# Kernel optimization log

Hardware: AMD Instinct MI355X
Metric: run time of the kernel (lower is better)

The kernel has to match this reference:

```python
import jax, jax.numpy as jnp
import numpy as np

B, S, HID = 4, 2048, 1152
H, KV, D = 16, 8, 72
NDIM = 2
EPS = 1e-6


def rms_norm(x, w, eps=EPS):
    # Gemma-style: normalize in fp32, scale by (1 + w)
    var = jnp.mean(jnp.square(x.astype(jnp.float32)), axis=-1, keepdims=True)
    y = x.astype(jnp.float32) * jax.lax.rsqrt(var + eps)
    if w is not None:
        y = y * (1.0 + w.astype(jnp.float32))
    return y.astype(x.dtype)


def rotate_half(x):
    x1, x2 = jnp.split(x, 2, axis=-1)
    return jnp.concatenate([-x2, x1], axis=-1)


def multidim_rope(x, cos, sin, ndim=NDIM):
    # x: [B, S, h, D]; cos/sin: [B, S, D]; rotate per spatial axis on D//ndim chunks
    part = 2 * (x.shape[-1] // (2 * ndim))  # 36
    outs = []
    for i in range(ndim):
        sl = slice(i * part, (i + 1) * part)
        xp = x[..., sl]
        c = cos[..., sl][:, :, None, :]  # unsqueeze head dim
        s = sin[..., sl][:, :, None, :]
        outs.append(xp * c + rotate_half(xp) * s)
    return jnp.concatenate(outs, axis=-1)


def setup_inputs() -> dict:
    key = jax.random.key(0)
    ks = jax.random.split(key, 10)
    inv = 1.0 / np.sqrt(HID)
    return {
        "hidden_states": jax.random.normal(ks[0], (B, S, HID), jnp.float32),
        "cos": jax.random.uniform(ks[1], (B, S, D), jnp.float32),
        "sin": jax.random.uniform(ks[2], (B, S, D), jnp.float32),
        "attention_mask": jnp.zeros((B, 1, S, S), jnp.float32),
        "position_ids": jax.random.randint(ks[3], (B, S, NDIM), 0, 64, jnp.int32),
        "Wq": jax.random.normal(ks[4], (HID, H * D), jnp.float32) * inv,
        "Wk": jax.random.normal(ks[5], (HID, KV * D), jnp.float32) * inv,
        "Wv": jax.random.normal(ks[6], (HID, KV * D), jnp.float32) * inv,
        "Wo": jax.random.normal(ks[7], (H * D, HID), jnp.float32) * inv,
        "q_norm_w": jnp.zeros((D,), jnp.float32),
        "k_norm_w": jnp.zeros((D,), jnp.float32),
    }


def reference(hidden_states, cos, sin, attention_mask, position_ids,
              Wq, Wk, Wv, Wo, q_norm_w, k_norm_w):
    ndim = position_ids.shape[-1]
    groups = H // KV
    # projections -> [B, S, h, D]
    q = (hidden_states @ Wq).reshape(B, S, H, D)
    k = (hidden_states @ Wk).reshape(B, S, KV, D)
    v = (hidden_states @ Wv).reshape(B, S, KV, D)
    # per-head RMSNorm
    q = rms_norm(q, q_norm_w)
    k = rms_norm(k, k_norm_w)
    v = rms_norm(v, None)  # with_scale=False
    # split multidimensional RoPE
    q = multidim_rope(q, cos, sin, ndim)
    k = multidim_rope(k, cos, sin, ndim)
    # GQA: repeat kv heads
    k = jnp.repeat(k, groups, axis=2)  # [B, S, H, D]
    v = jnp.repeat(v, groups, axis=2)
    # attention (note: source applies NO 1/sqrt(D) scaling)
    scores = jnp.einsum("bqhd,bkhd->bhqk", q, k) + attention_mask
    probs = jax.nn.softmax(scores.astype(jnp.float32), axis=-1).astype(q.dtype)
    out = jnp.einsum("bhqk,bkhd->bqhd", probs, v).reshape(B, S, H * D)
    return out @ Wo
```

## Files before the change

### kernel.cpp

```cpp
#include <hip/hip_runtime.h>

typedef unsigned int u32;
typedef unsigned short u16;
typedef __attribute__((ext_vector_type(8))) short s8v;
typedef __attribute__((ext_vector_type(8))) __bf16 b8v;
typedef __attribute__((ext_vector_type(4))) float f4v;
typedef __attribute__((ext_vector_type(16))) float f32x16;
typedef __attribute__((ext_vector_type(4))) u32 u32x4;
typedef __attribute__((ext_vector_type(2))) u32 u32x2;

#define DEV static __device__ __forceinline__

DEV u32 cvtpk(float a, float b){ u32 r; asm("v_cvt_pk_bf16_f32 %0, %1, %2" : "=v"(r) : "v"(a), "v"(b)); return r; }
DEV u16 f2bf(float x){ return (u16)(cvtpk(x, x) & 0xffffu); }
DEV float bf2f(u16 u){ return __builtin_bit_cast(float, ((u32)u) << 16); }

DEV f4v mfma16(s8v a, s8v b, f4v c){
  return __builtin_amdgcn_mfma_f32_16x16x32_bf16(__builtin_bit_cast(b8v, a), __builtin_bit_cast(b8v, b), c, 0, 0, 0);
}
DEV f32x16 mfma32(s8v a, s8v b, f32x16 c){
  return __builtin_amdgcn_mfma_f32_32x32x16_bf16(__builtin_bit_cast(b8v, a), __builtin_bit_cast(b8v, b), c, 0, 0, 0);
}

DEV void gl_lds16(const void* g, void* l){
  __builtin_amdgcn_global_load_lds((const __attribute__((address_space(1))) u32*)g,
                                   (__attribute__((address_space(3))) u32*)l, 16, 0, 0);
}

__global__ __launch_bounds__(256) void k_prepx(const float* __restrict__ x, u16* __restrict__ xb, int n){
  int i = (blockIdx.x * 256 + threadIdx.x) * 8;
  if (i >= n) return;
  float4 a = *(const float4*)(x + i);
  float4 b = *(const float4*)(x + i + 4);
  u32x4 o;
  o.x = cvtpk(a.x, a.y); o.y = cvtpk(a.z, a.w);
  o.z = cvtpk(b.x, b.y); o.w = cvtpk(b.z, b.w);
  *(u32x4*)(xb + i) = o;
}

__global__ __launch_bounds__(256) void k_transpose(const float* __restrict__ src, u16* __restrict__ dst,
                                                   int K, int N, int ldd){
  __shared__ float t[32][33];
  int nt = N >> 5;
  int k0 = (blockIdx.x / nt) << 5, n0 = (blockIdx.x % nt) << 5;
  int col = threadIdx.x & 31, rw = threadIdx.x >> 5;
  #pragma unroll
  for (int i = 0; i < 4; i++){ int r = rw + i * 8; t[r][col] = src[(k0 + r) * N + n0 + col]; }
  __syncthreads();
  #pragma unroll
  for (int i = 0; i < 4; i++){ int r = rw + i * 8; dst[(n0 + r) * ldd + k0 + col] = f2bf(t[col][r]); }
}

template<int OUTF32>
__global__ __launch_bounds__(256) void k_gemm(const u16* __restrict__ A, const u16* __restrict__ Bt,
                                              void* __restrict__ Cv, int M, int N, int K){
  __shared__ u16 sA[128 * 64];
  __shared__ u16 sB[128 * 64];
  int tid = threadIdx.x, w = tid >> 6, lane = tid & 63, g = lane >> 4, c = lane & 15;
  int n0 = blockIdx.x << 7, m0 = blockIdx.y << 7;
  int wr = w >> 1, wc = w & 1;
  f4v acc[4][4] = {};
  int srow = lane >> 3;
  int sslot = (lane & 7) ^ srow;
  const u16* Abase = A + (m0 + srow) * K + sslot * 8;
  const u16* Bbase = Bt + (n0 + srow) * K + sslot * 8;
  #pragma unroll 1
  for (int kt = 0; kt < K; kt += 64){
    #pragma unroll
    for (int ii = 0; ii < 4; ii++){
      int i = w * 4 + ii;
      gl_lds16(Abase + i * 8 * K + kt, sA + i * 512);
      gl_lds16(Bbase + i * 8 * K + kt, sB + i * 512);
    }
    __syncthreads();
    #pragma unroll
    for (int kk = 0; kk < 2; kk++){
      s8v af[4], bfr[4];
      #pragma unroll
      for (int mi = 0; mi < 4; mi++){
        int r = (wr << 6) + (mi << 4) + c;
        int slot = ((kk << 2) + g) ^ (r & 7);
        af[mi] = *(const s8v*)(sA + r * 64 + slot * 8);
      }
      #pragma unroll
      for (int ni = 0; ni < 4; ni++){
        int r = (wc << 6) + (ni << 4) + c;
        int slot = ((kk << 2) + g) ^ (r & 7);
        bfr[ni] = *(const s8v*)(sB + r * 64 + slot * 8);
      }
      #pragma unroll
      for (int mi = 0; mi < 4; mi++)
        #pragma unroll
        for (int ni = 0; ni < 4; ni++)
          acc[mi][ni] = mfma16(af[mi], bfr[ni], acc[mi][ni]);
    }
    __syncthreads();
  }
  #pragma unroll
  for (int mi = 0; mi < 4; mi++){
    #pragma unroll
    for (int ni = 0; ni < 4; ni++){
      #pragma unroll
      for (int r = 0; r < 4; r++){
        int m = m0 + (wr << 6) + (mi << 4) + (g << 2) + r;
        int n = n0 + (wc << 6) + (ni << 4) + c;
        if (OUTF32) ((float*)Cv)[m * N + n] = acc[mi][ni][r];
        else        ((u16*)Cv)[m * N + n] = f2bf(acc[mi][ni][r]);
      }
    }
  }
}

__global__ __launch_bounds__(192) void k_normrope(const u16* __restrict__ Y, const float* __restrict__ cosp,
      const float* __restrict__ sinp, const float* __restrict__ qnw, const float* __restrict__ knw,
      u16* __restrict__ Qp, u16* __restrict__ Kp){
  __shared__ float ly[1728];
  int token = blockIdx.x;
  int t = threadIdx.x, head = t >> 3, j = t & 7;
  int base = head * 72 + j * 9;
  const u16* yr = Y + token * 2304;
  float x[9]; float ss = 0.f;
  #pragma unroll
  for (int i = 0; i < 9; i++){ x[i] = bf2f(yr[base + i]); ss += x[i] * x[i]; }
  ss += __shfl_xor(ss, 1); ss += __shfl_xor(ss, 2); ss += __shfl_xor(ss, 4);
  float inv = rsqrtf(ss * (1.f / 72.f) + 1e-6f);
  const float* wn = (head < 16) ? qnw : knw;
  #pragma unroll
  for (int i = 0; i < 9; i++){ int d = j * 9 + i; ly[base + i] = x[i] * inv * (1.f + wn[d]); }
  __syncthreads();
  const float* cs = cosp + token * 72;
  const float* sn = sinp + token * 72;
  float scale = (head < 16) ? 1.4426950408889634f : 1.0f;
  float o[9];
  #pragma unroll
  for (int i = 0; i < 9; i++){
    int d = j * 9 + i;
    int dm = (d >= 36) ? d - 36 : d;
    float rot = (dm < 18) ? -ly[head * 72 + d + 18] : ly[head * 72 + d - 18];
    o[i] = (ly[base + i] * cs[d] + rot * sn[d]) * scale;
  }
  int b = token >> 11, s = token & 2047;
  if (head < 16){
    u16* dst = Qp + (size_t)(((b << 4) + head) * 2048 + s) * 96;
    #pragma unroll
    for (int i = 0; i < 9; i++) dst[j * 9 + i] = f2bf(o[i]);
    #pragma unroll
    for (int p2 = 0; p2 < 3; p2++) dst[72 + j * 3 + p2] = 0;
  } else {
    u16* dst = Kp + (size_t)(((b << 3) + (head - 16)) * 2048 + s) * 128;
    #pragma unroll
    for (int i = 0; i < 9; i++) dst[j * 9 + i] = f2bf(o[i]);
    #pragma unroll
    for (int p2 = 0; p2 < 7; p2++) dst[72 + j * 7 + p2] = 0;
  }
}

__global__ __launch_bounds__(256) void k_vtrans(const u16* __restrict__ Y, u16* __restrict__ Vt){
  __shared__ float lv[72][33];
  int st = blockIdx.x, bk = blockIdx.y;
  int b = bk >> 3, kvh = bk & 7;
  int t = threadIdx.x, tl = t >> 3, j = t & 7;
  int token = (b << 11) + (st << 5) + tl;
  const u16* yr = Y + token * 2304 + 1728 + kvh * 72 + j * 9;
  float x[9]; float ss = 0.f;
  #pragma unroll
  for (int i = 0; i < 9; i++){ x[i] = bf2f(yr[i]); ss += x[i] * x[i]; }
  ss += __shfl_xor(ss, 1); ss += __shfl_xor(ss, 2); ss += __shfl_xor(ss, 4);
  float inv = rsqrtf(ss * (1.f / 72.f) + 1e-6f);
  #pragma unroll
  for (int i = 0; i < 9; i++) lv[j * 9 + i][tl] = x[i] * inv;
  __syncthreads();
  u16* vb = Vt + bk * 72 * 2048 + (st << 5);
  for (int e = t; e < 72 * 32; e += 256){
    int r = e >> 5, cl = e & 31;
    vb[r * 2048 + cl] = f2bf(lv[r][cl]);
  }
}

__global__ __launch_bounds__(512, 4) void k_attn(const u16* __restrict__ Qp, const u16* __restrict__ Kp,
                                                 const u16* __restrict__ Vt, u16* __restrict__ O){
  __shared__ u16 sK[2][64 * 128];
  __shared__ u16 sV[2][96 * 64];
  int tid = threadIdx.x, w = tid >> 6, lane = tid & 63, hi = lane >> 5, l31 = lane & 31;
  int qt = blockIdx.x, bh = blockIdx.y, b = bh >> 4, h = bh & 15, kv = h >> 1;
  int q = (qt << 8) + (w << 5) + l31;
  const u16* qb = Qp + (size_t)((((b << 4) + h) << 11) + q) * 96;
  s8v qf[5];
  #pragma unroll
  for (int ds = 0; ds < 5; ds++) qf[ds] = *(const s8v*)(qb + ds * 16 + hi * 8);
  f32x16 ao[3] = {};
  float mv = -3.0e38f, lsp = 0.f;
  const char* kb = (const char*)Kp + (((size_t)((b << 3) + kv)) << 11) * 256;
  const char* vb = (const char*)Vt + (size_t)((b << 3) + kv) * 72 * 4096;
  int kn0 = (0 * 8 + w) * 64 + lane, kn1 = (1 * 8 + w) * 64 + lane;
  int kr0 = kn0 >> 4, kr1 = kn1 >> 4;
  int ksrc0 = kr0 * 256 + (((lane & 15) ^ (kr0 & 15)) << 4);
  int ksrc1 = kr1 * 256 + (((lane & 15) ^ (kr1 & 15)) << 4);
  int kdst0 = kn0 << 4, kdst1 = kn1 << 4;
  int vn0 = w * 64 + lane, vn1 = 512 + lane;
  int vr0 = vn0 >> 3, vr1 = vn1 >> 3;
  int vsrc0 = vr0 * 4096 + (((lane & 7) ^ (vr0 & 7)) << 4);
  int vsrc1 = vr1 * 4096 + (((lane & 7) ^ (vr1 & 7)) << 4);
  int vdst0 = vn0 << 4, vdst1 = vn1 << 4;

#define STAGE_KV(buf, t1) { \
    const char* kt_ = kb + (size_t)(t1) * 16384; \
    gl_lds16(kt_ + ksrc0, (char*)sK[buf] + kdst0); \
    gl_lds16(kt_ + ksrc1, (char*)sK[buf] + kdst1); \
    const char* vt_ = vb + (size_t)(t1) * 128; \
    gl_lds16(vt_ + vsrc0, (char*)sV[buf] + vdst0); \
    if (w == 0) gl_lds16(vt_ + vsrc1, (char*)sV[buf] + vdst1); }

  STAGE_KV(0, 0)
  __syncthreads();

  #pragma unroll 1
  for (int t = 0; t < 32; t++){
    int cur = t & 1, nxt = cur ^ 1;
    if (t < 31){ STAGE_KV(nxt, t + 1) }
    const u16* sKc = sK[cur];
    f32x16 s0 = {}, s1 = {};
    __builtin_amdgcn_s_setprio(1);
    #pragma unroll
    for (int ds = 0; ds < 5; ds++){
      int s = ds * 2 + hi;
      int r0 = l31, r1 = 32 + l31;
      s8v k0 = *(const s8v*)(sKc + r0 * 128 + ((s ^ (r0 & 15)) << 3));
      s8v k1 = *(const s8v*)(sKc + r1 * 128 + ((s ^ (r1 & 15)) << 3));
      s0 = mfma32(k0, qf[ds], s0);
      s1 = mfma32(k1, qf[ds], s1);
    }
    __builtin_amdgcn_s_setprio(0);
    float tm = s0[0];
    #pragma unroll
    for (int i = 1; i < 16; i++) tm = fmaxf(tm, s0[i]);
    #pragma unroll
    for (int i = 0; i < 16; i++) tm = fmaxf(tm, s1[i]);
    tm = fmaxf(tm, __shfl_xor(tm, 32));
    if (!__all(tm <= mv + 8.f)){
      float mn = fmaxf(mv, tm);
      float scl = exp2f(mv - mn);
      lsp *= scl;
      ao[0] *= scl; ao[1] *= scl; ao[2] *= scl;
      mv = mn;
    }
    float ts = 0.f;
    #pragma unroll
    for (int i = 0; i < 16; i++){ float e = exp2f(s0[i] - mv); s0[i] = e; ts += e; }
    #pragma unroll
    for (int i = 0; i < 16; i++){ float e = exp2f(s1[i] - mv); s1[i] = e; ts += e; }
    lsp += ts;
    s8v pf[4];
#define MK_PF(S, ks) { \
      const int blo = ((ks) & 1) * 8; \
      u32 a0 = cvtpk(S[blo + 0], S[blo + 1]); \
      u32 a1 = cvtpk(S[blo + 2], S[blo + 3]); \
      u32 b0 = cvtpk(S[blo + 4], S[blo + 5]); \
      u32 b1 = cvtpk(S[blo + 6], S[blo + 7]); \
      asm("v_permlane32_swap_b32 %0, %1" : "+v"(a0), "+v"(b0)); \
      asm("v_permlane32_swap_b32 %0, %1" : "+v"(a1), "+v"(b1)); \
      u32x4 w4 = {a0, a1, b0, b1}; \
      pf[ks] = __builtin_bit_cast(s8v, w4); }
    MK_PF(s0, 0) MK_PF(s0, 1) MK_PF(s1, 2) MK_PF(s1, 3)
#undef MK_PF
    const u16* sVc = sV[cur];
    __builtin_amdgcn_s_setprio(1);
    #pragma unroll
    for (int ks = 0; ks < 4; ks++){
      int s = ks * 2 + hi;
      #pragma unroll
      for (int dt = 0; dt < 3; dt++){
        int r = dt * 32 + l31;
        s8v vf = *(const s8v*)(sVc + r * 64 + ((s ^ (r & 7)) << 3));
        ao[dt] = mfma32(vf, pf[ks], ao[dt]);
      }
    }
    __builtin_amdgcn_s_setprio(0);
    __syncthreads();
  }
  float ls = lsp + __shfl_xor(lsp, 32);
  float inv = 1.f / ls;
  u16* ob = O + (size_t)((((b << 11) + q) << 4) + h) * 72;
  #pragma unroll
  for (int dt = 0; dt < 3; dt++){
    #pragma unroll
    for (int gp = 0; gp < 4; gp++){
      int d = dt * 32 + gp * 8 + hi * 4;
      if (d < 72){
        u32x2 o2;
        o2.x = cvtpk(ao[dt][gp * 4 + 0] * inv, ao[dt][gp * 4 + 1] * inv);
        o2.y = cvtpk(ao[dt][gp * 4 + 2] * inv, ao[dt][gp * 4 + 3] * inv);
        *(u32x2*)(ob + d) = o2;
      }
    }
  }
#undef STAGE_KV
}

extern "C" void kernel_launch(void* const* d_in, const int* in_sizes, int n_in,
                              void* d_out, int out_size, void* d_ws, size_t ws_size,
                              hipStream_t stream){
  (void)in_sizes; (void)n_in; (void)out_size; (void)ws_size;
  const float* hs   = (const float*)d_in[0];
  const float* cosp = (const float*)d_in[1];
  const float* sinp = (const float*)d_in[2];
  const float* Wq   = (const float*)d_in[5];
  const float* Wk   = (const float*)d_in[6];
  const float* Wv   = (const float*)d_in[7];
  const float* Wo   = (const float*)d_in[8];
  const float* qnw  = (const float*)d_in[9];
  const float* knw  = (const float*)d_in[10];
  char* ws = (char*)d_ws;
  u16* Xb    = (u16*)(ws);
  u16* WtQKV = (u16*)(ws + 18874368);
  u16* Wot   = (u16*)(ws + 24182784);
  u16* Y     = (u16*)(ws + 26836992);
  u16* Qp    = (u16*)(ws + 64585728);
  u16* Kp    = (u16*)(ws + 89751552);
  u16* Vt    = (u16*)(ws + 106528768);
  u16* O     = Xb;

  k_prepx<<<4608, 256, 0, stream>>>(hs, Xb, 8192 * 1152);
  k_transpose<<<36 * 36, 256, 0, stream>>>(Wq, WtQKV, 1152, 1152, 1152);
  k_transpose<<<36 * 18, 256, 0, stream>>>(Wk, WtQKV + 1152 * 1152, 1152, 576, 1152);
  k_transpose<<<36 * 18, 256, 0, stream>>>(Wv, WtQKV + 1728 * 1152, 1152, 576, 1152);
  k_transpose<<<36 * 36, 256, 0, stream>>>(Wo, Wot, 1152, 1152, 1152);
  k_gemm<0><<<dim3(18, 64), 256, 0, stream>>>(Xb, WtQKV, Y, 8192, 2304, 1152);
  k_normrope<<<8192, 192, 0, stream>>>(Y, cosp, sinp, qnw, knw, Qp, Kp);
  k_vtrans<<<dim3(64, 32), 256, 0, stream>>>(Y, Vt);
  k_attn<<<dim3(8, 64), 512, 0, stream>>>(Qp, Kp, Vt, O);
  k_gemm<1><<<dim3(9, 64), 256, 0, stream>>>(O, Wot, (float*)d_out, 8192, 1152, 1152);
}
```

Before: 324.9 us.

## Share KV tiles across GQA head pair and double KV tile to 128

Each attention block now serves both query heads that share one KV head (4 waves per head, 128 queries each), so the staged K/V tiles in LDS are reused by two heads and global KV traffic halves. The KV tile grows from 64 to 128 keys per iteration, halving loop trips and barriers, with the LDS swizzle rewritten for 128-wide V rows. This raises LDS use and register pressure (four score accumulators), and launch bounds drop to 2 blocks per CU, which reduces occupancy.

```diff
diff --git a/kernel.cpp b/kernel.cpp
--- a/kernel.cpp
+++ b/kernel.cpp
@@ -177,65 +177,78 @@
   }
 }
 
-__global__ __launch_bounds__(512, 4) void k_attn(const u16* __restrict__ Qp, const u16* __restrict__ Kp,
+__global__ __launch_bounds__(512, 2) void k_attn(const u16* __restrict__ Qp, const u16* __restrict__ Kp,
                                                  const u16* __restrict__ Vt, u16* __restrict__ O){
-  __shared__ u16 sK[2][64 * 128];
-  __shared__ u16 sV[2][96 * 64];
+  __shared__ u16 sK[2][128 * 128];
+  __shared__ u16 sV[2][96 * 128];
   int tid = threadIdx.x, w = tid >> 6, lane = tid & 63, hi = lane >> 5, l31 = lane & 31;
-  int qt = blockIdx.x, bh = blockIdx.y, b = bh >> 4, h = bh & 15, kv = h >> 1;
-  int q = (qt << 8) + (w << 5) + l31;
+  int bk = blockIdx.x, qt = blockIdx.y;
+  int b = bk >> 3, kv = bk & 7;
+  int h = (kv << 1) + (w >> 2);
+  int q = (qt << 7) + ((w & 3) << 5) + l31;
   const u16* qb = Qp + (size_t)((((b << 4) + h) << 11) + q) * 96;
   s8v qf[5];
   #pragma unroll
   for (int ds = 0; ds < 5; ds++) qf[ds] = *(const s8v*)(qb + ds * 16 + hi * 8);
   f32x16 ao[3] = {};
   float mv = -3.0e38f, lsp = 0.f;
-  const char* kb = (const char*)Kp + (((size_t)((b << 3) + kv)) << 11) * 256;
-  const char* vb = (const char*)Vt + (size_t)((b << 3) + kv) * 72 * 4096;
-  int kn0 = (0 * 8 + w) * 64 + lane, kn1 = (1 * 8 + w) * 64 + lane;
-  int kr0 = kn0 >> 4, kr1 = kn1 >> 4;
-  int ksrc0 = kr0 * 256 + (((lane & 15) ^ (kr0 & 15)) << 4);
-  int ksrc1 = kr1 * 256 + (((lane & 15) ^ (kr1 & 15)) << 4);
-  int kdst0 = kn0 << 4, kdst1 = kn1 << 4;
-  int vn0 = w * 64 + lane, vn1 = 512 + lane;
-  int vr0 = vn0 >> 3, vr1 = vn1 >> 3;
-  int vsrc0 = vr0 * 4096 + (((lane & 7) ^ (vr0 & 7)) << 4);
-  int vsrc1 = vr1 * 4096 + (((lane & 7) ^ (vr1 & 7)) << 4);
-  int vdst0 = vn0 << 4, vdst1 = vn1 << 4;
-
-#define STAGE_KV(buf, t1) { \
-    const char* kt_ = kb + (size_t)(t1) * 16384; \
-    gl_lds16(kt_ + ksrc0, (char*)sK[buf] + kdst0); \
-    gl_lds16(kt_ + ksrc1, (char*)sK[buf] + kdst1); \
-    const char* vt_ = vb + (size_t)(t1) * 128; \
-    gl_lds16(vt_ + vsrc0, (char*)sV[buf] + vdst0); \
-    if (w == 0) gl_lds16(vt_ + vsrc1, (char*)sV[buf] + vdst1); }
-
-  STAGE_KV(0, 0)
+  const char* kb = (const char*)Kp + (size_t)bk * 2048 * 256;
+  const char* vb = (const char*)Vt + (size_t)bk * 72 * 4096;
+  int ko[4], kd[4];
+  #pragma unroll
+  for (int i = 0; i < 4; i++){
+    int n = (i * 8 + w) * 64 + lane;
+    int kr = n >> 4, sp = n & 15;
+    ko[i] = kr * 256 + ((sp ^ (kr & 15)) << 4);
+    kd[i] = n << 4;
+  }
+  int vo[3], vd[3];
+  #pragma unroll
+  for (int i = 0; i < 3; i++){
+    int n = (i < 2) ? (i * 512 + w * 64 + lane) : (1024 + w * 16 + (lane & 15));
+    int vr = n >> 4, sp = n & 15;
+    vo[i] = vr * 4096 + ((sp ^ (vr & 15)) << 4);
+    vd[i] = n << 4;
+  }
+
+#define STAGE(buf, t1) { \
+    const char* kt_ = kb + (size_t)(t1) * 32768; \
+    gl_lds16(kt_ + ko[0], (char*)sK[buf] + kd[0]); \
+    gl_lds16(kt_ + ko[1], (char*)sK[buf] + kd[1]); \
+    gl_lds16(kt_ + ko[2], (char*)sK[buf] + kd[2]); \
+    gl_lds16(kt_ + ko[3], (char*)sK[buf] + kd[3]); \
+    const char* vt_ = vb + (size_t)(t1) * 256; \
+    gl_lds16(vt_ + vo[0], (char*)sV[buf] + vd[0]); \
+    gl_lds16(vt_ + vo[1], (char*)sV[buf] + vd[1]); \
+    if (lane < 16) gl_lds16(vt_ + vo[2], (char*)sV[buf] + vd[2]); }
+
+  STAGE(0, 0)
   __syncthreads();
 
   #pragma unroll 1
-  for (int t = 0; t < 32; t++){
+  for (int t = 0; t < 16; t++){
     int cur = t & 1, nxt = cur ^ 1;
-    if (t < 31){ STAGE_KV(nxt, t + 1) }
+    if (t < 15){ STAGE(nxt, t + 1) }
     const u16* sKc = sK[cur];
-    f32x16 s0 = {}, s1 = {};
+    f32x16 sc[4];
     __builtin_amdgcn_s_setprio(1);
     #pragma unroll
-    for (int ds = 0; ds < 5; ds++){
-      int s = ds * 2 + hi;
-      int r0 = l31, r1 = 32 + l31;
-      s8v k0 = *(const s8v*)(sKc + r0 * 128 + ((s ^ (r0 & 15)) << 3));
-      s8v k1 = *(const s8v*)(sKc + r1 * 128 + ((s ^ (r1 & 15)) << 3));
-      s0 = mfma32(k0, qf[ds], s0);
-      s1 = mfma32(k1, qf[ds], s1);
+    for (int j = 0; j < 4; j++){
+      sc[j] = {};
+      int r = j * 32 + l31;
+      #pragma unroll
+      for (int ds = 0; ds < 5; ds++){
+        int s = ds * 2 + hi;
+        s8v kf = *(const s8v*)(sKc + r * 128 + ((s ^ (r & 15)) << 3));
+        sc[j] = mfma32(kf, qf[ds], sc[j]);
+      }
     }
     __builtin_amdgcn_s_setprio(0);
-    float tm = s0[0];
-    #pragma unroll
-    for (int i = 1; i < 16; i++) tm = fmaxf(tm, s0[i]);
-    #pragma unroll
-    for (int i = 0; i < 16; i++) tm = fmaxf(tm, s1[i]);
+    float tm = sc[0][0];
+    #pragma unroll
+    for (int j = 0; j < 4; j++)
+      #pragma unroll
+      for (int i = 0; i < 16; i++) tm = fmaxf(tm, sc[j][i]);
     tm = fmaxf(tm, __shfl_xor(tm, 32));
     if (!__all(tm <= mv + 8.f)){
       float mn = fmaxf(mv, tm);
@@ -244,38 +257,43 @@
       ao[0] *= scl; ao[1] *= scl; ao[2] *= scl;
       mv = mn;
     }
-    float ts = 0.f;
-    #pragma unroll
-    for (int i = 0; i < 16; i++){ float e = exp2f(s0[i] - mv); s0[i] = e; ts += e; }
-    #pragma unroll
-    for (int i = 0; i < 16; i++){ float e = exp2f(s1[i] - mv); s1[i] = e; ts += e; }
-    lsp += ts;
-    s8v pf[4];
-#define MK_PF(S, ks) { \
-      const int blo = ((ks) & 1) * 8; \
-      u32 a0 = cvtpk(S[blo + 0], S[blo + 1]); \
-      u32 a1 = cvtpk(S[blo + 2], S[blo + 3]); \
-      u32 b0 = cvtpk(S[blo + 4], S[blo + 5]); \
-      u32 b1 = cvtpk(S[blo + 6], S[blo + 7]); \
+    float ts0 = 0.f, ts1 = 0.f;
+    #pragma unroll
+    for (int j = 0; j < 4; j++){
+      #pragma unroll
+      for (int i = 0; i < 8; i++){ float e = exp2f(sc[j][i] - mv); sc[j][i] = e; ts0 += e; }
+      #pragma unroll
+      for (int i = 8; i < 16; i++){ float e = exp2f(sc[j][i] - mv); sc[j][i] = e; ts1 += e; }
+    }
+    lsp += ts0 + ts1;
+    const u16* sVc = sV[cur];
+#define MK_PF(S, mlo, PF) { \
+      u32 a0 = cvtpk(S[mlo + 0], S[mlo + 1]); \
+      u32 a1 = cvtpk(S[mlo + 2], S[mlo + 3]); \
+      u32 b0 = cvtpk(S[mlo + 4], S[mlo + 5]); \
+      u32 b1 = cvtpk(S[mlo + 6], S[mlo + 7]); \
       asm("v_permlane32_swap_b32 %0, %1" : "+v"(a0), "+v"(b0)); \
       asm("v_permlane32_swap_b32 %0, %1" : "+v"(a1), "+v"(b1)); \
       u32x4 w4 = {a0, a1, b0, b1}; \
-      pf[ks] = __builtin_bit_cast(s8v, w4); }
-    MK_PF(s0, 0) MK_PF(s0, 1) MK_PF(s1, 2) MK_PF(s1, 3)
-#undef MK_PF
-    const u16* sVc = sV[cur];
-    __builtin_amdgcn_s_setprio(1);
-    #pragma unroll
-    for (int ks = 0; ks < 4; ks++){
-      int s = ks * 2 + hi;
+      PF = __builtin_bit_cast(s8v, w4); }
+    #pragma unroll
+    for (int j = 0; j < 4; j++){
+      s8v pfa, pfb;
+      MK_PF(sc[j], 0, pfa)
+      MK_PF(sc[j], 8, pfb)
+      __builtin_amdgcn_s_setprio(1);
       #pragma unroll
       for (int dt = 0; dt < 3; dt++){
         int r = dt * 32 + l31;
-        s8v vf = *(const s8v*)(sVc + r * 64 + ((s ^ (r & 7)) << 3));
-        ao[dt] = mfma32(vf, pf[ks], ao[dt]);
-      }
-    }
-    __builtin_amdgcn_s_setprio(0);
+        int s0 = 4 * j + hi, s1 = 4 * j + 2 + hi;
+        s8v vf0 = *(const s8v*)(sVc + r * 128 + ((s0 ^ (r & 15)) << 3));
+        s8v vf1 = *(const s8v*)(sVc + r * 128 + ((s1 ^ (r & 15)) << 3));
+        ao[dt] = mfma32(vf0, pfa, ao[dt]);
+        ao[dt] = mfma32(vf1, pfb, ao[dt]);
+      }
+      __builtin_amdgcn_s_setprio(0);
+    }
+#undef MK_PF
     __syncthreads();
   }
   float ls = lsp + __shfl_xor(lsp, 32);
@@ -294,7 +312,7 @@
       }
     }
   }
-#undef STAGE_KV
+#undef STAGE
 }
 
 extern "C" void kernel_launch(void* const* d_in, const int* in_sizes, int n_in,
@@ -328,6 +346,6 @@
   k_gemm<0><<<dim3(18, 64), 256, 0, stream>>>(Xb, WtQKV, Y, 8192, 2304, 1152);
   k_normrope<<<8192, 192, 0, stream>>>(Y, cosp, sinp, qnw, knw, Qp, Kp);
   k_vtrans<<<dim3(64, 32), 256, 0, stream>>>(Y, Vt);
-  k_attn<<<dim3(8, 64), 512, 0, stream>>>(Qp, Kp, Vt, O);
+  k_attn<<<dim3(32, 16), 512, 0, stream>>>(Qp, Kp, Vt, O);
   k_gemm<1><<<dim3(9, 64), 256, 0, stream>>>(O, Wot, (float*)d_out, 8192, 1152, 1152);
 }
```

After: 316.5 us. 2.6% less time.
